# Performance work log

Measured on AMD Instinct MI355X. Metric: run time of the kernel, lower is better.

The kernel has to match this reference:

```python
import jax, jax.numpy as jnp
import numpy as np

E, D, H, N = 8, 1024, 4096, 8192  # experts, model dim, moe intermediate, total tokens


def setup_inputs() -> dict:
    key = jax.random.key(0)
    k0, k1, k2, k3 = jax.random.split(key, 4)
    x = jax.random.normal(k0, (N, D), jnp.float32)
    # PrimeRL layout: w1,w3: [E, H, D]; w2: [E, D, H]
    w1 = jax.random.normal(k1, (E, H, D), jnp.float32) * 0.02
    w2 = jax.random.normal(k2, (E, D, H), jnp.float32) * 0.02
    w3 = jax.random.normal(k3, (E, H, D), jnp.float32) * 0.02
    num_tokens_per_expert = jnp.full((E,), N // E, dtype=jnp.int32)  # balanced, sums to N
    return {"x": x, "w1": w1, "w2": w2, "w3": w3,
            "num_tokens_per_expert": num_tokens_per_expert}


def reference(x, w1, w2, w3, num_tokens_per_expert):
    # grouped MoE FFN: per expert e over its contiguous token block,
    #   h = gelu_tanh(x @ w1[e].T) * (x @ w3[e].T); out = h @ w2[e].T
    # torch path casts to bf16 for the grouped mm, casts output back.
    gs = num_tokens_per_expert.astype(jnp.int32)  # group sizes = offsets via cumsum
    xb = x.astype(jnp.bfloat16)
    w1t = jnp.swapaxes(w1, -2, -1).astype(jnp.bfloat16)  # [E, D, H]
    w2t = jnp.swapaxes(w2, -2, -1).astype(jnp.bfloat16)  # [E, H, D]
    w3t = jnp.swapaxes(w3, -2, -1).astype(jnp.bfloat16)  # [E, D, H]
    g = jax.lax.ragged_dot(xb, w1t, gs)                  # [N, H]
    h = jax.nn.gelu(g, approximate=True) * jax.lax.ragged_dot(xb, w3t, gs)
    out = jax.lax.ragged_dot(h, w2t, gs).astype(x.dtype)  # [N, D]
    return out
```

## Files before the change

### kernel.cpp

```cpp
#include <hip/hip_runtime.h>
#include <hip/hip_bf16.h>

#define E_ 8
#define D_ 1024
#define H_ 4096
#define N_ 8192

typedef __attribute__((ext_vector_type(8))) short bf16x8;
typedef __attribute__((ext_vector_type(4))) float f32x4;
typedef unsigned short u16;

static __device__ __forceinline__ u16 f2bf(float f) {
    unsigned int u = __float_as_uint(f);
    u += 0x7fffu + ((u >> 16) & 1u);
    return (u16)(u >> 16);
}

static __device__ __forceinline__ void st_bf4(u16* p, float4 v) {
    union { u16 u[4]; unsigned long long ll; } t;
    t.u[0] = f2bf(v.x); t.u[1] = f2bf(v.y); t.u[2] = f2bf(v.z); t.u[3] = f2bf(v.w);
    *(unsigned long long*)p = t.ll;
}

static __device__ __forceinline__ float gelu_tanh(float x) {
    float x3 = x * x * x;
    float z = 0.7978845608028654f * (x + 0.044715f * x3);
    float t = 1.0f - 2.0f / (1.0f + __expf(2.0f * z));
    return 0.5f * x * (1.0f + t);
}

static __device__ __forceinline__ int expert_of(const int* __restrict__ ntpe, int row) {
    int acc = 0;
    #pragma unroll
    for (int i = 0; i < E_; ++i) {
        acc += ntpe[i];
        if (row < acc) return i;
    }
    return E_ - 1;
}

#define GLD16(gp, lp) __builtin_amdgcn_global_load_lds( \
    (const __attribute__((address_space(1))) void*)(gp), \
    (__attribute__((address_space(3))) void*)(lp), 16, 0, 0)

__global__ __launch_bounds__(256) void cvt_all(
    const float* __restrict__ x, const float* __restrict__ w1,
    const float* __restrict__ w2, const float* __restrict__ w3,
    u16* __restrict__ xb, u16* __restrict__ w1b,
    u16* __restrict__ w2b, u16* __restrict__ w3b)
{
    const float* srcs[4] = {x, w1, w2, w3};
    u16* dsts[4] = {xb, w1b, w2b, w3b};
    const int cnt4[4] = {N_ * D_ / 4, E_ * H_ * D_ / 4, E_ * D_ * H_ / 4, E_ * H_ * D_ / 4};
    int gtid = blockIdx.x * 256 + threadIdx.x;
    int gstride = gridDim.x * 256;
    #pragma unroll
    for (int s = 0; s < 4; ++s) {
        const float4* src = (const float4*)srcs[s];
        u16* dst = dsts[s];
        for (int i = gtid; i < cnt4[s]; i += gstride) {
            float4 v = src[i];
            st_bf4(dst + (size_t)i * 4, v);
        }
    }
}

__global__ __launch_bounds__(256, 2) void moe_gemm13_fast(
    const u16* __restrict__ xb, const u16* __restrict__ w1b,
    const u16* __restrict__ w3b, const int* __restrict__ ntpe,
    u16* __restrict__ hbuf)
{
    __shared__ u16 sA[128 * 32], sB1[128 * 32], sB2[128 * 32];
    const int tid = threadIdx.x;
    const int m0 = blockIdx.y * 128, n0 = blockIdx.x * 128;
    const int e = expert_of(ntpe, m0);
    const int wave = tid >> 6, lane = tid & 63;
    const int wm = (wave >> 1) * 64, wn = (wave & 1) * 64;
    const int fr = lane & 15, quad = lane >> 4;

    const u16* Ag  = xb  + (size_t)m0 * D_;
    const u16* B1g = w1b + ((size_t)e * H_ + n0) * D_;
    const u16* B2g = w3b + ((size_t)e * H_ + n0) * D_;

    const int srow = wave * 32 + (lane >> 2);
    const int scol = (lane & 3) * 8;

    f32x4 accg[4][4], accu[4][4];
    #pragma unroll
    for (int i = 0; i < 4; ++i)
        #pragma unroll
        for (int j = 0; j < 4; ++j) {
            accg[i][j] = (f32x4){0.f, 0.f, 0.f, 0.f};
            accu[i][j] = (f32x4){0.f, 0.f, 0.f, 0.f};
        }

    for (int k0 = 0; k0 < D_; k0 += 32) {
        #pragma unroll
        for (int c = 0; c < 2; ++c) {
            size_t go = (size_t)(srow + c * 16) * D_ + k0 + scol;
            int lb = (wave * 2 + c) * 16 * 32;
            GLD16(Ag + go,  &sA[lb]);
            GLD16(B1g + go, &sB1[lb]);
            GLD16(B2g + go, &sB2[lb]);
        }
        __syncthreads();

        bf16x8 fa[4], fb1[4], fb2[4];
        #pragma unroll
        for (int i = 0; i < 4; ++i) {
            fa[i]  = *(const bf16x8*)(&sA [(wm + i * 16 + fr) * 32 + quad * 8]);
            fb1[i] = *(const bf16x8*)(&sB1[(wn + i * 16 + fr) * 32 + quad * 8]);
            fb2[i] = *(const bf16x8*)(&sB2[(wn + i * 16 + fr) * 32 + quad * 8]);
        }
        #pragma unroll
        for (int i = 0; i < 4; ++i)
            #pragma unroll
            for (int j = 0; j < 4; ++j) {
                accg[i][j] = __builtin_amdgcn_mfma_f32_16x16x32_bf16(fa[i], fb1[j], accg[i][j], 0, 0, 0);
                accu[i][j] = __builtin_amdgcn_mfma_f32_16x16x32_bf16(fa[i], fb2[j], accu[i][j], 0, 0, 0);
            }
        __syncthreads();
    }

    #pragma unroll
    for (int i = 0; i < 4; ++i) {
        int rowb = m0 + wm + i * 16 + quad * 4;
        #pragma unroll
        for (int j = 0; j < 4; ++j) {
            int col = n0 + wn + j * 16 + fr;
            #pragma unroll
            for (int r = 0; r < 4; ++r) {
                float hv = gelu_tanh(accg[i][j][r]) * accu[i][j][r];
                hbuf[(size_t)(rowb + r) * H_ + col] = f2bf(hv);
            }
        }
    }
}

__global__ __launch_bounds__(256, 2) void moe_gemm2_fast(
    const u16* __restrict__ hbuf, const u16* __restrict__ w2b,
    const int* __restrict__ ntpe, float* __restrict__ out)
{
    __shared__ u16 sA[128 * 32], sB[128 * 32];
    const int tid = threadIdx.x;
    const int m0 = blockIdx.y * 128, n0 = blockIdx.x * 128;
    const int e = expert_of(ntpe, m0);
    const int wave = tid >> 6, lane = tid & 63;
    const int wm = (wave >> 1) * 64, wn = (wave & 1) * 64;
    const int fr = lane & 15, quad = lane >> 4;

    const u16* Ag = hbuf + (size_t)m0 * H_;
    const u16* Bg = w2b + ((size_t)e * D_ + n0) * H_;

    const int srow = wave * 32 + (lane >> 2);
    const int scol = (lane & 3) * 8;

    f32x4 acc[4][4];
    #pragma unroll
    for (int i = 0; i < 4; ++i)
        #pragma unroll
        for (int j = 0; j < 4; ++j)
            acc[i][j] = (f32x4){0.f, 0.f, 0.f, 0.f};

    for (int k0 = 0; k0 < H_; k0 += 32) {
        #pragma unroll
        for (int c = 0; c < 2; ++c) {
            size_t go = (size_t)(srow + c * 16) * H_ + k0 + scol;
            int lb = (wave * 2 + c) * 16 * 32;
            GLD16(Ag + go, &sA[lb]);
            GLD16(Bg + go, &sB[lb]);
        }
        __syncthreads();

        bf16x8 fa[4], fb[4];
        #pragma unroll
        for (int i = 0; i < 4; ++i) {
            fa[i] = *(const bf16x8*)(&sA[(wm + i * 16 + fr) * 32 + quad * 8]);
            fb[i] = *(const bf16x8*)(&sB[(wn + i * 16 + fr) * 32 + quad * 8]);
        }
        #pragma unroll
        for (int i = 0; i < 4; ++i)
            #pragma unroll
            for (int j = 0; j < 4; ++j)
                acc[i][j] = __builtin_amdgcn_mfma_f32_16x16x32_bf16(fa[i], fb[j], acc[i][j], 0, 0, 0);
        __syncthreads();
    }

    #pragma unroll
    for (int i = 0; i < 4; ++i) {
        int rowb = m0 + wm + i * 16 + quad * 4;
        #pragma unroll
        for (int j = 0; j < 4; ++j) {
            int col = n0 + wn + j * 16 + fr;
            #pragma unroll
            for (int r = 0; r < 4; ++r)
                out[(size_t)(rowb + r) * D_ + col] = acc[i][j][r];
        }
    }
}

#define LDSP 40

__global__ __launch_bounds__(256, 2) void moe_gemm13_slow(
    const float* __restrict__ x, const float* __restrict__ w1,
    const float* __restrict__ w3, const int* __restrict__ ntpe,
    u16* __restrict__ hbuf)
{
    const int tid = threadIdx.x;
    const int m0 = blockIdx.y * 128, n0 = blockIdx.x * 128;
    const int e = expert_of(ntpe, m0);
    __shared__ u16 sA[128][LDSP]; __shared__ u16 sB1[128][LDSP]; __shared__ u16 sB2[128][LDSP];
    const int wave = tid >> 6, lane = tid & 63;
    const int wm = (wave >> 1) * 64, wn = (wave & 1) * 64;
    const int fr = lane & 15, quad = lane >> 4;
    f32x4 accg[4][4], accu[4][4];
    #pragma unroll
    for (int i = 0; i < 4; ++i)
        #pragma unroll
        for (int j = 0; j < 4; ++j) {
            accg[i][j] = (f32x4){0.f,0.f,0.f,0.f}; accu[i][j] = (f32x4){0.f,0.f,0.f,0.f};
        }
    const float* Ab  = x  + (size_t)m0 * D_;
    const float* B1b = w1 + ((size_t)e * H_ + n0) * D_;
    const float* B2b = w3 + ((size_t)e * H_ + n0) * D_;
    for (int k0 = 0; k0 < D_; k0 += 32) {
        #pragma unroll
        for (int s = 0; s < 4; ++s) {
            int idx = s * 256 + tid;
            int row = idx >> 3, col = (idx & 7) * 4;
            size_t go = (size_t)row * D_ + k0 + col;
            st_bf4(&sA[row][col],  *(const float4*)(Ab + go));
            st_bf4(&sB1[row][col], *(const float4*)(B1b + go));
            st_bf4(&sB2[row][col], *(const float4*)(B2b + go));
        }
        __syncthreads();
        bf16x8 fa[4], fb1[4], fb2[4];
        #pragma unroll
        for (int i = 0; i < 4; ++i) {
            fa[i]  = *(const bf16x8*)(&sA[wm + i * 16 + fr][quad * 8]);
            fb1[i] = *(const bf16x8*)(&sB1[wn + i * 16 + fr][quad * 8]);
            fb2[i] = *(const bf16x8*)(&sB2[wn + i * 16 + fr][quad * 8]);
        }
        #pragma unroll
        for (int i = 0; i < 4; ++i)
            #pragma unroll
            for (int j = 0; j < 4; ++j) {
                accg[i][j] = __builtin_amdgcn_mfma_f32_16x16x32_bf16(fa[i], fb1[j], accg[i][j], 0, 0, 0);
                accu[i][j] = __builtin_amdgcn_mfma_f32_16x16x32_bf16(fa[i], fb2[j], accu[i][j], 0, 0, 0);
            }
        __syncthreads();
    }
    #pragma unroll
    for (int i = 0; i < 4; ++i) {
        int rowb = m0 + wm + i * 16 + quad * 4;
        #pragma unroll
        for (int j = 0; j < 4; ++j) {
            int col = n0 + wn + j * 16 + fr;
            #pragma unroll
            for (int r = 0; r < 4; ++r)
                hbuf[(size_t)(rowb + r) * H_ + col] = f2bf(gelu_tanh(accg[i][j][r]) * accu[i][j][r]);
        }
    }
}

__global__ __launch_bounds__(256, 2) void moe_gemm2_slow(
    const u16* __restrict__ hbuf, const float* __restrict__ w2,
    const int* __restrict__ ntpe, float* __restrict__ out)
{
    const int tid = threadIdx.x;
    const int m0 = blockIdx.y * 128, n0 = blockIdx.x * 128;
    const int e = expert_of(ntpe, m0);
    __shared__ u16 sA[128][LDSP]; __shared__ u16 sB[128][LDSP];
    const int wave = tid >> 6, lane = tid & 63;
    const int wm = (wave >> 1) * 64, wn = (wave & 1) * 64;
    const int fr = lane & 15, quad = lane >> 4;
    f32x4 acc[4][4];
    #pragma unroll
    for (int i = 0; i < 4; ++i)
        #pragma unroll
        for (int j = 0; j < 4; ++j) acc[i][j] = (f32x4){0.f,0.f,0.f,0.f};
    const u16* Ab = hbuf + (size_t)m0 * H_;
    const float* Bb = w2 + ((size_t)e * D_ + n0) * H_;
    for (int k0 = 0; k0 < H_; k0 += 32) {
        #pragma unroll
        for (int s = 0; s < 2; ++s) {
            int idx = s * 256 + tid;
            int row = idx >> 2, col = (idx & 3) * 8;
            *(bf16x8*)(&sA[row][col]) = *(const bf16x8*)(Ab + (size_t)row * H_ + k0 + col);
        }
        #pragma unroll
        for (int s = 0; s < 4; ++s) {
            int idx = s * 256 + tid;
            int row = idx >> 3, col = (idx & 7) * 4;
            st_bf4(&sB[row][col], *(const float4*)(Bb + (size_t)row * H_ + k0 + col));
        }
        __syncthreads();
        bf16x8 fa[4], fb[4];
        #pragma unroll
        for (int i = 0; i < 4; ++i) {
            fa[i] = *(const bf16x8*)(&sA[wm + i * 16 + fr][quad * 8]);
            fb[i] = *(const bf16x8*)(&sB[wn + i * 16 + fr][quad * 8]);
        }
        #pragma unroll
        for (int i = 0; i < 4; ++i)
            #pragma unroll
            for (int j = 0; j < 4; ++j)
                acc[i][j] = __builtin_amdgcn_mfma_f32_16x16x32_bf16(fa[i], fb[j], acc[i][j], 0, 0, 0);
        __syncthreads();
    }
    #pragma unroll
    for (int i = 0; i < 4; ++i) {
        int rowb = m0 + wm + i * 16 + quad * 4;
        #pragma unroll
        for (int j = 0; j < 4; ++j) {
            int col = n0 + wn + j * 16 + fr;
            #pragma unroll
            for (int r = 0; r < 4; ++r)
                out[(size_t)(rowb + r) * D_ + col] = acc[i][j][r];
        }
    }
}

extern "C" void kernel_launch(void* const* d_in, const int* in_sizes, int n_in,
                              void* d_out, int out_size, void* d_ws, size_t ws_size,
                              hipStream_t stream) {
    const float* x  = (const float*)d_in[0];
    const float* w1 = (const float*)d_in[1];
    const float* w2 = (const float*)d_in[2];
    const float* w3 = (const float*)d_in[3];
    const int* ntpe = (const int*)d_in[4];
    float* out = (float*)d_out;

    const size_t SZ_XB = (size_t)N_ * D_ * 2;
    const size_t SZ_W  = (size_t)E_ * H_ * D_ * 2;
    const size_t SZ_H  = (size_t)N_ * H_ * 2;
    const size_t NEED  = SZ_XB + 3 * SZ_W + SZ_H;

    if (ws_size >= NEED) {
        char* p = (char*)d_ws;
        u16* xb  = (u16*)p;                 p += SZ_XB;
        u16* w1b = (u16*)p;                 p += SZ_W;
        u16* w3b = (u16*)p;                 p += SZ_W;
        u16* w2b = (u16*)p;                 p += SZ_W;
        u16* hb  = (u16*)p;

        cvt_all<<<4096, 256, 0, stream>>>(x, w1, w2, w3, xb, w1b, w2b, w3b);

        dim3 g1(H_ / 128, N_ / 128);
        moe_gemm13_fast<<<g1, 256, 0, stream>>>(xb, w1b, w3b, ntpe, hb);

        dim3 g2(D_ / 128, N_ / 128);
        moe_gemm2_fast<<<g2, 256, 0, stream>>>(hb, w2b, ntpe, out);
    } else {
        u16* hb = (u16*)d_ws;
        dim3 g1(H_ / 128, N_ / 128);
        moe_gemm13_slow<<<g1, 256, 0, stream>>>(x, w1, w3, ntpe, hb);
        dim3 g2(D_ / 128, N_ / 128);
        moe_gemm2_slow<<<g2, 256, 0, stream>>>(hb, w2, ntpe, out);
    }
}
```

Before: 740.1 us.

## Narrow gate/up GEMM tile, stage epilogue through LDS, split conversion per tensor

The fused gate/up GEMM tile shrinks from 128x128 to 128x64 per block. This halves the accumulator registers so launch bounds can ask for 3 blocks per CU. The epilogue now writes GELU*up results into padded shared memory and then stores 16-byte coalesced rows instead of scattered 2-byte writes. The fp32-to-bf16 conversion kernel gives each tensor its own block range and writes 8 elements per store. The narrower tile re-reads the x tile twice as often. gemm2 also gets the 3-block launch bound, which may force register spills.

```diff
diff --git a/kernel.cpp b/kernel.cpp
--- a/kernel.cpp
+++ b/kernel.cpp
@@ -43,79 +43,97 @@
     (const __attribute__((address_space(1))) void*)(gp), \
     (__attribute__((address_space(3))) void*)(lp), 16, 0, 0)
 
-__global__ __launch_bounds__(256) void cvt_all(
+#define CVT_XBLK 512
+#define CVT_WBLK 2048
+#define CVT_NBLK (CVT_XBLK + 3 * CVT_WBLK)
+
+__global__ __launch_bounds__(256) void cvt_all2(
     const float* __restrict__ x, const float* __restrict__ w1,
     const float* __restrict__ w2, const float* __restrict__ w3,
     u16* __restrict__ xb, u16* __restrict__ w1b,
     u16* __restrict__ w2b, u16* __restrict__ w3b)
 {
-    const float* srcs[4] = {x, w1, w2, w3};
-    u16* dsts[4] = {xb, w1b, w2b, w3b};
-    const int cnt4[4] = {N_ * D_ / 4, E_ * H_ * D_ / 4, E_ * D_ * H_ / 4, E_ * H_ * D_ / 4};
-    int gtid = blockIdx.x * 256 + threadIdx.x;
-    int gstride = gridDim.x * 256;
-    #pragma unroll
-    for (int s = 0; s < 4; ++s) {
-        const float4* src = (const float4*)srcs[s];
-        u16* dst = dsts[s];
-        for (int i = gtid; i < cnt4[s]; i += gstride) {
-            float4 v = src[i];
-            st_bf4(dst + (size_t)i * 4, v);
-        }
-    }
-}
-
-__global__ __launch_bounds__(256, 2) void moe_gemm13_fast(
+    int b = blockIdx.x;
+    const float* src; u16* dst; int n8; int b0; int nb;
+    if (b < CVT_XBLK) {
+        src = x; dst = xb; n8 = N_ * D_ / 8; b0 = 0; nb = CVT_XBLK;
+    } else if (b < CVT_XBLK + CVT_WBLK) {
+        src = w1; dst = w1b; n8 = E_ * H_ * D_ / 8; b0 = CVT_XBLK; nb = CVT_WBLK;
+    } else if (b < CVT_XBLK + 2 * CVT_WBLK) {
+        src = w2; dst = w2b; n8 = E_ * D_ * H_ / 8; b0 = CVT_XBLK + CVT_WBLK; nb = CVT_WBLK;
+    } else {
+        src = w3; dst = w3b; n8 = E_ * H_ * D_ / 8; b0 = CVT_XBLK + 2 * CVT_WBLK; nb = CVT_WBLK;
+    }
+    int t = (b - b0) * 256 + threadIdx.x;
+    int stride = nb * 256;
+    const float4* s4 = (const float4*)src;
+    for (int i = t; i < n8; i += stride) {
+        float4 a = s4[i * 2];
+        float4 c = s4[i * 2 + 1];
+        union { u16 u[8]; bf16x8 v; } o;
+        o.u[0] = f2bf(a.x); o.u[1] = f2bf(a.y); o.u[2] = f2bf(a.z); o.u[3] = f2bf(a.w);
+        o.u[4] = f2bf(c.x); o.u[5] = f2bf(c.y); o.u[6] = f2bf(c.z); o.u[7] = f2bf(c.w);
+        *(bf16x8*)(dst + (size_t)i * 8) = o.v;
+    }
+}
+
+#define EPIT 72
+
+__global__ __launch_bounds__(256, 3) void moe_gemm13_fast(
     const u16* __restrict__ xb, const u16* __restrict__ w1b,
     const u16* __restrict__ w3b, const int* __restrict__ ntpe,
     u16* __restrict__ hbuf)
 {
-    __shared__ u16 sA[128 * 32], sB1[128 * 32], sB2[128 * 32];
+    __shared__ u16 smem[128 * EPIT];
+    u16* sA  = smem;
+    u16* sB1 = smem + 4096;
+    u16* sB2 = smem + 6144;
+
     const int tid = threadIdx.x;
-    const int m0 = blockIdx.y * 128, n0 = blockIdx.x * 128;
+    const int m0 = blockIdx.y * 128, n0 = blockIdx.x * 64;
     const int e = expert_of(ntpe, m0);
     const int wave = tid >> 6, lane = tid & 63;
-    const int wm = (wave >> 1) * 64, wn = (wave & 1) * 64;
+    const int wm = (wave >> 1) * 64, wn = (wave & 1) * 32;
     const int fr = lane & 15, quad = lane >> 4;
 
     const u16* Ag  = xb  + (size_t)m0 * D_;
     const u16* B1g = w1b + ((size_t)e * H_ + n0) * D_;
     const u16* B2g = w3b + ((size_t)e * H_ + n0) * D_;
 
-    const int srow = wave * 32 + (lane >> 2);
+    const int srA = wave * 32 + (lane >> 2);
+    const int srB = wave * 16 + (lane >> 2);
     const int scol = (lane & 3) * 8;
 
-    f32x4 accg[4][4], accu[4][4];
+    f32x4 accg[4][2], accu[4][2];
     #pragma unroll
     for (int i = 0; i < 4; ++i)
         #pragma unroll
-        for (int j = 0; j < 4; ++j) {
+        for (int j = 0; j < 2; ++j) {
             accg[i][j] = (f32x4){0.f, 0.f, 0.f, 0.f};
             accu[i][j] = (f32x4){0.f, 0.f, 0.f, 0.f};
         }
 
     for (int k0 = 0; k0 < D_; k0 += 32) {
         #pragma unroll
-        for (int c = 0; c < 2; ++c) {
-            size_t go = (size_t)(srow + c * 16) * D_ + k0 + scol;
-            int lb = (wave * 2 + c) * 16 * 32;
-            GLD16(Ag + go,  &sA[lb]);
-            GLD16(B1g + go, &sB1[lb]);
-            GLD16(B2g + go, &sB2[lb]);
-        }
-        __syncthreads();
-
-        bf16x8 fa[4], fb1[4], fb2[4];
-        #pragma unroll
-        for (int i = 0; i < 4; ++i) {
-            fa[i]  = *(const bf16x8*)(&sA [(wm + i * 16 + fr) * 32 + quad * 8]);
-            fb1[i] = *(const bf16x8*)(&sB1[(wn + i * 16 + fr) * 32 + quad * 8]);
-            fb2[i] = *(const bf16x8*)(&sB2[(wn + i * 16 + fr) * 32 + quad * 8]);
-        }
-        #pragma unroll
-        for (int i = 0; i < 4; ++i)
-            #pragma unroll
-            for (int j = 0; j < 4; ++j) {
+        for (int c = 0; c < 2; ++c)
+            GLD16(Ag + (size_t)(srA + c * 16) * D_ + k0 + scol, sA + (wave * 32 + c * 16) * 32);
+        GLD16(B1g + (size_t)srB * D_ + k0 + scol, sB1 + wave * 16 * 32);
+        GLD16(B2g + (size_t)srB * D_ + k0 + scol, sB2 + wave * 16 * 32);
+        __syncthreads();
+
+        bf16x8 fa[4], fb1[2], fb2[2];
+        #pragma unroll
+        for (int i = 0; i < 4; ++i)
+            fa[i] = *(const bf16x8*)(&sA[(wm + i * 16 + fr) * 32 + quad * 8]);
+        #pragma unroll
+        for (int j = 0; j < 2; ++j) {
+            fb1[j] = *(const bf16x8*)(&sB1[(wn + j * 16 + fr) * 32 + quad * 8]);
+            fb2[j] = *(const bf16x8*)(&sB2[(wn + j * 16 + fr) * 32 + quad * 8]);
+        }
+        #pragma unroll
+        for (int i = 0; i < 4; ++i)
+            #pragma unroll
+            for (int j = 0; j < 2; ++j) {
                 accg[i][j] = __builtin_amdgcn_mfma_f32_16x16x32_bf16(fa[i], fb1[j], accg[i][j], 0, 0, 0);
                 accu[i][j] = __builtin_amdgcn_mfma_f32_16x16x32_bf16(fa[i], fb2[j], accu[i][j], 0, 0, 0);
             }
@@ -124,20 +142,29 @@
 
     #pragma unroll
     for (int i = 0; i < 4; ++i) {
-        int rowb = m0 + wm + i * 16 + quad * 4;
-        #pragma unroll
-        for (int j = 0; j < 4; ++j) {
-            int col = n0 + wn + j * 16 + fr;
+        int rl = wm + i * 16 + quad * 4;
+        #pragma unroll
+        for (int j = 0; j < 2; ++j) {
+            int cl = wn + j * 16 + fr;
             #pragma unroll
             for (int r = 0; r < 4; ++r) {
                 float hv = gelu_tanh(accg[i][j][r]) * accu[i][j][r];
-                hbuf[(size_t)(rowb + r) * H_ + col] = f2bf(hv);
+                smem[(rl + r) * EPIT + cl] = f2bf(hv);
             }
         }
     }
-}
-
-__global__ __launch_bounds__(256, 2) void moe_gemm2_fast(
+    __syncthreads();
+    #pragma unroll
+    for (int it = 0; it < 4; ++it) {
+        int chunk = it * 256 + tid;
+        int row = chunk >> 3;
+        int col = (chunk & 7) * 8;
+        bf16x8 v = *(const bf16x8*)(&smem[row * EPIT + col]);
+        *(bf16x8*)(&hbuf[(size_t)(m0 + row) * H_ + n0 + col]) = v;
+    }
+}
+
+__global__ __launch_bounds__(256, 3) void moe_gemm2_fast(
     const u16* __restrict__ hbuf, const u16* __restrict__ w2b,
     const int* __restrict__ ntpe, float* __restrict__ out)
 {
@@ -344,9 +371,9 @@
         u16* w2b = (u16*)p;                 p += SZ_W;
         u16* hb  = (u16*)p;
 
-        cvt_all<<<4096, 256, 0, stream>>>(x, w1, w2, w3, xb, w1b, w2b, w3b);
-
-        dim3 g1(H_ / 128, N_ / 128);
+        cvt_all2<<<CVT_NBLK, 256, 0, stream>>>(x, w1, w2, w3, xb, w1b, w2b, w3b);
+
+        dim3 g1(H_ / 64, N_ / 128);
         moe_gemm13_fast<<<g1, 256, 0, stream>>>(xb, w1b, w3b, ntpe, hb);
 
         dim3 g2(D_ / 128, N_ / 128);
```

New measurement: 705.5 us. -4.7%, faster.
